# Kernel optimization log

Measured on AMD Instinct MI355X. Metric: run time of the kernel, lower is better.

The kernel has to match this reference:

```python
import jax, jax.numpy as jnp
import numpy as np

V, E, HL, HH, T_STEPS, N_STEPS = 32000, 768, 1024, 768, 5, 3
B, S = 8, 256
EPS = 1e-5


def _ln(x, g, b):
    m = jnp.mean(x, axis=-1, keepdims=True)
    v = jnp.var(x, axis=-1, keepdims=True)
    return (x - m) * jax.lax.rsqrt(v + EPS) * g + b


def _gru(x, h, Wi, bi, Wh, bh, lni_g, lni_b, lnh_g, lnh_b):
    # Wi: [3, in_dim, H]; gates stacked in order (r, z, n)
    xi = jnp.einsum('bd,kdh->kbh', x, Wi) + bi[:, None, :]
    hi = jnp.einsum('bh,khg->kbg', h, Wh) + bh[:, None, :]
    xi = _ln(xi, lni_g[:, None, :], lni_b[:, None, :])
    hi = _ln(hi, lnh_g[:, None, :], lnh_b[:, None, :])
    r = jax.nn.sigmoid(xi[0] + hi[0])
    z = jax.nn.sigmoid(xi[1] + hi[1])
    n = jnp.tanh(xi[2] + r * hi[2])
    return (1.0 - z) * n + z * h


def setup_inputs() -> dict:
    key = jax.random.key(0)
    ks = jax.random.split(key, 12)
    lin = E + HH  # low-level cell input dim (x concat h_h)

    def xavier(k, shape, fan_in, fan_out):
        lim = float(np.sqrt(6.0 / (fan_in + fan_out)))
        return jax.random.uniform(k, shape, jnp.float32, -lim, lim)

    inp = {
        'input_ids': jax.random.randint(ks[0], (B, S), 0, V),
        'emb': xavier(ks[1], (V, E), V, E),
        'ln_emb_g': jnp.ones((E,), jnp.float32),
        'ln_emb_b': jnp.zeros((E,), jnp.float32),
        'low_Wi': xavier(ks[2], (3, lin, HL), lin, HL),
        'low_bi': jnp.zeros((3, HL), jnp.float32),
        'low_Wh': xavier(ks[3], (3, HL, HL), HL, HL),
        'low_bh': jnp.zeros((3, HL), jnp.float32),
        'low_lni_g': jnp.ones((3, HL), jnp.float32),
        'low_lni_b': jnp.zeros((3, HL), jnp.float32),
        'low_lnh_g': jnp.ones((3, HL), jnp.float32),
        'low_lnh_b': jnp.zeros((3, HL), jnp.float32),
        'high_Wi': xavier(ks[4], (3, HL, HH), HL, HH),
        'high_bi': jnp.zeros((3, HH), jnp.float32),
        'high_Wh': xavier(ks[5], (3, HH, HH), HH, HH),
        'high_bh': jnp.zeros((3, HH), jnp.float32),
        'high_lni_g': jnp.ones((3, HH), jnp.float32),
        'high_lni_b': jnp.zeros((3, HH), jnp.float32),
        'high_lnh_g': jnp.ones((3, HH), jnp.float32),
        'high_lnh_b': jnp.zeros((3, HH), jnp.float32),
        'Wout': xavier(ks[6], (HH, V), HH, V),
        'bout': jnp.zeros((V,), jnp.float32),
    }
    return inp


def reference(input_ids, emb, ln_emb_g, ln_emb_b,
              low_Wi, low_bi, low_Wh, low_bh,
              low_lni_g, low_lni_b, low_lnh_g, low_lnh_b,
              high_Wi, high_bi, high_Wh, high_bh,
              high_lni_g, high_lni_b, high_lnh_g, high_lnh_b,
              Wout, bout):
    b = input_ids.shape[0]
    h_l0 = jnp.zeros((b, HL), jnp.float32)
    h_h0 = jnp.zeros((b, HH), jnp.float32)

    def step(carry, ids_t):
        h_l, h_h = carry
        x = _ln(emb[ids_t], ln_emb_g, ln_emb_b)  # [B, E]
        for _ in range(N_STEPS):
            for _ in range(T_STEPS):
                h_l = _gru(jnp.concatenate([x, h_h], axis=-1), h_l,
                           low_Wi, low_bi, low_Wh, low_bh,
                           low_lni_g, low_lni_b, low_lnh_g, low_lnh_b)
            h_h = _gru(h_l, h_h,
                       high_Wi, high_bi, high_Wh, high_bh,
                       high_lni_g, high_lni_b, high_lnh_g, high_lnh_b)
        logits_t = h_h @ Wout + bout  # [B, V]
        return (h_l, h_h), logits_t

    _, logits = jax.lax.scan(step, (h_l0, h_h0), input_ids.T)  # [S, B, V]
    return jnp.transpose(logits, (1, 0, 2))  # [B, S, V]
```

## Files before the change

kernel.cpp:

```cpp
#include <hip/hip_runtime.h>
#include <hip/hip_bf16.h>


#define NWG 128
#define NTH 256
#define EPSV 1e-5f
#define NROUND 4608

typedef __attribute__((ext_vector_type(4))) float f32x4;
typedef __attribute__((ext_vector_type(8))) short short8;
typedef unsigned long long u64;

struct PArgs {
  const int* ids; const float* emb; const float* lng; const float* lnb;
  const float* lWi; const float* lbi; const float* lWh; const float* lbh;
  const float* llig; const float* llib; const float* llhg; const float* llhb;
  const float* hWi; const float* hbi; const float* hWh; const float* hbh;
  const float* hlig; const float* hlib; const float* hlhg; const float* hlhb;
  int* arr; int* rel; int* cnt; u64* sredG; u64* statsG; float* hlR; float* hhR;
  __hip_bfloat16* hist; float* WiT; float* hWiT; float* hWhT;
};

__device__ __forceinline__ float sigm(float x) { return 1.f / (1.f + __expf(-x)); }
__device__ __forceinline__ float tanh_f(float x) {
  x = fminf(15.f, fmaxf(-15.f, x));
  float e = __expf(2.f * x);
  return (e - 1.f) / (e + 1.f);
}
__device__ __forceinline__ int aldi(const int* p) {
  return __hip_atomic_load(p, __ATOMIC_RELAXED, __HIP_MEMORY_SCOPE_AGENT);
}
__device__ __forceinline__ u64 aldu(const u64* p) {
  return __hip_atomic_load(p, __ATOMIC_RELAXED, __HIP_MEMORY_SCOPE_AGENT);
}
__device__ __forceinline__ void asti(int* p, int v) {
  __hip_atomic_store(p, v, __ATOMIC_RELAXED, __HIP_MEMORY_SCOPE_AGENT);
}
__device__ __forceinline__ u64 pk2(float a, float b) {
  union { u64 u; float f[2]; } c; c.f[0] = a; c.f[1] = b; return c.u;
}
__device__ __forceinline__ void astu(u64* p, u64 v) {
  __hip_atomic_store(p, v, __ATOMIC_RELAXED, __HIP_MEMORY_SCOPE_AGENT);
}
__device__ __forceinline__ void ast(float* p, float v) {
  __hip_atomic_store(p, v, __ATOMIC_RELAXED, __HIP_MEMORY_SCOPE_AGENT);
}
__device__ __forceinline__ void ald4x8(const float* p0, const float* p1,
                                       const float* p2, const float* p3,
                                       const float* p4, const float* p5,
                                       const float* p6, const float* p7,
                                       float4& a, float4& b, float4& c, float4& d,
                                       float4& e, float4& f, float4& g, float4& h) {
  asm volatile(
      "global_load_dwordx4 %0, %8, off sc1\n\t"
      "global_load_dwordx4 %1, %9, off sc1\n\t"
      "global_load_dwordx4 %2, %10, off sc1\n\t"
      "global_load_dwordx4 %3, %11, off sc1\n\t"
      "global_load_dwordx4 %4, %12, off sc1\n\t"
      "global_load_dwordx4 %5, %13, off sc1\n\t"
      "global_load_dwordx4 %6, %14, off sc1\n\t"
      "global_load_dwordx4 %7, %15, off sc1\n\t"
      "s_waitcnt vmcnt(0)"
      : "=&v"(a), "=&v"(b), "=&v"(c), "=&v"(d),
        "=&v"(e), "=&v"(f), "=&v"(g), "=&v"(h)
      : "v"(p0), "v"(p1), "v"(p2), "v"(p3),
        "v"(p4), "v"(p5), "v"(p6), "v"(p7)
      : "memory");
}
__device__ __forceinline__ void ald4x4(const float* p0, const float* p1,
                                       const float* p2, const float* p3,
                                       float4& a, float4& b, float4& c, float4& d) {
  asm volatile(
      "global_load_dwordx4 %0, %4, off sc1\n\t"
      "global_load_dwordx4 %1, %5, off sc1\n\t"
      "global_load_dwordx4 %2, %6, off sc1\n\t"
      "global_load_dwordx4 %3, %7, off sc1\n\t"
      "s_waitcnt vmcnt(0)"
      : "=&v"(a), "=&v"(b), "=&v"(c), "=&v"(d)
      : "v"(p0), "v"(p1), "v"(p2), "v"(p3)
      : "memory");
}
__device__ __forceinline__ void ald4x3(const float* p0, const float* p1,
                                       const float* p2,
                                       float4& a, float4& b, float4& c) {
  asm volatile(
      "global_load_dwordx4 %0, %3, off sc1\n\t"
      "global_load_dwordx4 %1, %4, off sc1\n\t"
      "global_load_dwordx4 %2, %5, off sc1\n\t"
      "s_waitcnt vmcnt(0)"
      : "=&v"(a), "=&v"(b), "=&v"(c)
      : "v"(p0), "v"(p1), "v"(p2)
      : "memory");
}

__global__ void __launch_bounds__(NTH) hrm_recur(PArgs P) {
  __shared__ float WhS[24 * 1024];
  __shared__ float Bb[8 * 1024];
  __shared__ float XW[24 * 8];
  __shared__ float xiNs[24 * 8];
  __shared__ float stg[2 * 24 * 8];
  __shared__ float sred[96];
  __shared__ float xm[8], xrs[8];
  __shared__ float mbuf[96][4];
  __shared__ int idsh[8];
  __shared__ int okf;

  const int tid = threadIdx.x;

  if (blockIdx.x >= NWG) {
    const int pl = blockIdx.x - NWG;
    #pragma unroll 1
    for (int r = 1; r <= NROUND; ++r) {
      if (tid < 64) {
        const u64* ap = (const u64*)(P.arr + pl * 128) + tid;
        int lim = 1 << 22, g1 = 1;
        for (;;) {
          u64 v = aldu(ap);
          int a0 = (int)(unsigned)(v & 0xffffffffull);
          int a1 = (int)(unsigned)(v >> 32);
          if (__all(a0 >= r && a1 >= r)) break;
          if (--lim == 0) { g1 = 0; break; }
          __builtin_amdgcn_s_sleep(1);
        }
        if (tid == 0) okf = g1;
      }
      __syncthreads();
      if (!okf) {
        if (tid < 8) asti(P.rel + pl * 128 + tid * 16, 1 << 30);
        return;
      }
      const int ph = (r - 1) % 6;
      const bool full = (ph == 0 || ph == 5);
      const int lo = pl * 24 + (full ? 0 : 12);
      const int n  = full ? 24 : 12;
      const float invD = (ph == 5) ? (1.f / 768.f) : (1.f / 1024.f);
      const int par = r & 1;
      if (tid < (n >> 1) * 8) {
        int rp = (lo >> 1) + (tid >> 3), q = tid & 7;
        const float* fb = (const float*)(P.statsG + (size_t)par * 128 * 48);
        float4 s; s.x = 0.f; s.y = 0.f; s.z = 0.f; s.w = 0.f;
        #pragma unroll
        for (int blk = 0; blk < 2; ++blk) {
          int w0 = q * 16 + blk * 8;
          float4 t0,t1,t2,t3,t4,t5,t6,t7;
          ald4x8(fb + (size_t)(w0+0)*96 + rp*4, fb + (size_t)(w0+1)*96 + rp*4,
                 fb + (size_t)(w0+2)*96 + rp*4, fb + (size_t)(w0+3)*96 + rp*4,
                 fb + (size_t)(w0+4)*96 + rp*4, fb + (size_t)(w0+5)*96 + rp*4,
                 fb + (size_t)(w0+6)*96 + rp*4, fb + (size_t)(w0+7)*96 + rp*4,
                 t0,t1,t2,t3,t4,t5,t6,t7);
          s.x += t0.x+t1.x+t2.x+t3.x+t4.x+t5.x+t6.x+t7.x;
          s.y += t0.y+t1.y+t2.y+t3.y+t4.y+t5.y+t6.y+t7.y;
          s.z += t0.z+t1.z+t2.z+t3.z+t4.z+t5.z+t6.z+t7.z;
          s.w += t0.w+t1.w+t2.w+t3.w+t4.w+t5.w+t6.w+t7.w;
        }
        mbuf[tid][0] = s.x; mbuf[tid][1] = s.y; mbuf[tid][2] = s.z; mbuf[tid][3] = s.w;
      }
      __syncthreads();
      if (tid < n) {
        int rpl = tid >> 1, comp = tid & 1;
        float s1 = 0.f, s2 = 0.f;
        #pragma unroll
        for (int q = 0; q < 8; ++q) {
          s1 += mbuf[rpl * 8 + q][comp * 2 + 0];
          s2 += mbuf[rpl * 8 + q][comp * 2 + 1];
        }
        float m = s1 * invD;
        float rs = rsqrtf(s2 * invD - m * m + EPSV);
        astu(P.sredG + (size_t)pl * 96 + (size_t)par * 48 + lo + tid, pk2(m, rs));
      }
      asm volatile("s_waitcnt vmcnt(0)" ::: "memory");
      __syncthreads();
      if (tid < 8) asti(P.rel + pl * 128 + tid * 16, r);
    }
    return;
  }

  const int wg = blockIdx.x;
  const int ks = tid & 31, cg = tid >> 5;
  const int lj8 = wg * 8, lj6 = wg * 6;
  const int rep = wg & 3;

  auto arriveA = [&](int pl, int r) {
    asm volatile("s_waitcnt vmcnt(0)" ::: "memory");
    __syncthreads();
    if (tid == 0) asti(P.arr + pl * 128 + wg, r);
  };
  auto pollRel = [&](int pl, int r, bool full) -> bool {
    if (tid == 0) {
      const int* rp = P.rel + pl * 128 + (wg & 7) * 16;
      int lim = 1 << 22, v = 0;
      do {
        v = aldi(rp);
        if (v >= r) break;
        __builtin_amdgcn_s_sleep(1);
      } while (--lim);
      okf = (lim != 0 && v < (1 << 29)) ? 1 : 0;
    }
    __syncthreads();
    if (okf) {
      int lo = pl * 24 + (full ? 0 : 12);
      int n  = full ? 24 : 12;
      if (tid < n) {
        int row = lo + tid;
        union { u64 u; float f[2]; } c;
        c.u = aldu(P.sredG + (size_t)pl * 96 + (size_t)(r & 1) * 48 + row);
        int local = row - pl * 24;
        int set = local / 12, rem = local % 12, g = rem >> 2, bq = rem & 3;
        int b = pl * 4 + bq;
        sred[set * 48 + g * 16 + b * 2] = c.f[0];
        sred[set * 48 + g * 16 + b * 2 + 1] = c.f[1];
      }
      __syncthreads();
    }
    return okf != 0;
  };
  auto waitB = [&](int pl, int target) -> bool {
    if (tid < 64) {
      bool active = tid < 8;
      const int* cp = P.cnt + pl * 256 + (size_t)(active ? tid : 0) * 32;
      int lim = 1 << 22;
      for (;;) {
        int v = active ? aldi(cp) : 0;
        int sum = v;
        sum += __shfl_xor(sum, 1);
        sum += __shfl_xor(sum, 2);
        sum += __shfl_xor(sum, 4);
        int total = __shfl(sum, 0);
        if (total >= target) break;
        if (--lim == 0) break;
        __builtin_amdgcn_s_sleep(2);
      }
      if (tid == 0) okf = (lim != 0) ? 1 : 0;
    }
    __syncthreads();
    return okf != 0;
  };
  auto gate_commit = [&](int pl) {
    asm volatile("s_waitcnt vmcnt(0)" ::: "memory");
    if (tid == 0)
      __hip_atomic_fetch_add(P.cnt + pl * 256 + (size_t)(wg & 7) * 32, 1,
                             __ATOMIC_RELAXED, __HIP_MEMORY_SCOPE_AGENT);
  };

  auto stage_hl = [&](int pl) {
    const float* base = P.hlR + (size_t)rep * 8192 + (size_t)pl * 4096 + tid * 4;
    float4 t0,t1,t2,t3;
    ald4x4(base + 0*1024, base + 1*1024, base + 2*1024, base + 3*1024,
           t0,t1,t2,t3);
    float* db = &Bb[pl * 4096 + tid * 4];
    *(float4*)&db[0*1024] = t0; *(float4*)&db[1*1024] = t1;
    *(float4*)&db[2*1024] = t2; *(float4*)&db[3*1024] = t3;
  };
  auto stage_hh = [&](int pl) {
    const float* base = P.hhR + (size_t)rep * 6144 + (size_t)pl * 3072;
    int bi[3], ki[3];
    #pragma unroll
    for (int i = 0; i < 3; ++i) {
      int c = i * 256 + tid; int bq = c / 192; int k = (c - bq * 192) * 4;
      bi[i] = bq; ki[i] = k;
    }
    float4 t0,t1,t2;
    ald4x3(base + bi[0]*768 + ki[0], base + bi[1]*768 + ki[1],
           base + bi[2]*768 + ki[2], t0,t1,t2);
    *(float4*)&Bb[(pl*4+bi[0])*1024 + ki[0]] = t0;
    *(float4*)&Bb[(pl*4+bi[1])*1024 + ki[1]] = t1;
    *(float4*)&Bb[(pl*4+bi[2])*1024 + ki[2]] = t2;
  };

  auto gemm_lowh = [&](int pl, float (&acc)[3][4]) {
    const int c0 = cg * 3;
    const float* w0p = &WhS[(c0 + 0) * 1024];
    const float* w1p = &WhS[(c0 + 1) * 1024];
    const float* w2p = &WhS[(c0 + 2) * 1024];
    const float* hb = &Bb[pl * 4096];
    #pragma unroll
    for (int i = 0; i < 8; ++i) {
      int k = i * 128 + ks * 4;
      float4 w0 = *(const float4*)&w0p[k];
      float4 w1 = *(const float4*)&w1p[k];
      float4 w2 = *(const float4*)&w2p[k];
      #pragma unroll
      for (int bq = 0; bq < 4; ++bq) {
        float4 h = *(const float4*)&hb[bq * 1024 + k];
        acc[0][bq] += w0.x*h.x + w0.y*h.y + w0.z*h.z + w0.w*h.w;
        acc[1][bq] += w1.x*h.x + w1.y*h.y + w1.z*h.z + w1.w*h.w;
        acc[2][bq] += w2.x*h.x + w2.y*h.y + w2.z*h.z + w2.w*h.w;
      }
    }
  };
  auto gemm_xih = [&](int pl, float (&acc)[3][4]) {
    const float* wp[3];
    #pragma unroll
    for (int cc = 0; cc < 3; ++cc) {
      int c = cg * 3 + cc; int g = c >> 3, jj = c & 7;
      wp[cc] = P.WiT + ((size_t)g * 1024 + lj8 + jj) * 1536 + 768;
    }
    const float* hb = &Bb[pl * 4096];
    #pragma unroll
    for (int i = 0; i < 6; ++i) {
      int k = i * 128 + ks * 4;
      float4 w0 = *(const float4*)&wp[0][k];
      float4 w1 = *(const float4*)&wp[1][k];
      float4 w2 = *(const float4*)&wp[2][k];
      #pragma unroll
      for (int bq = 0; bq < 4; ++bq) {
        float4 h = *(const float4*)&hb[bq * 1024 + k];
        acc[0][bq] += w0.x*h.x + w0.y*h.y + w0.z*h.z + w0.w*h.w;
        acc[1][bq] += w1.x*h.x + w1.y*h.y + w1.z*h.z + w1.w*h.w;
        acc[2][bq] += w2.x*h.x + w2.y*h.y + w2.z*h.z + w2.w*h.w;
      }
    }
  };
  auto gemm_hxi = [&](int pl, float (&acc)[3][4]) {
    if (cg >= 6) return;
    const float* wp[3];
    #pragma unroll
    for (int cc = 0; cc < 3; ++cc) {
      int c = cg * 3 + cc; int g = c / 6, jj = c % 6;
      wp[cc] = P.hWiT + ((size_t)g * 768 + lj6 + jj) * 1024;
    }
    const float* hb = &Bb[pl * 4096];
    #pragma unroll
    for (int i = 0; i < 8; ++i) {
      int k = i * 128 + ks * 4;
      float4 w0 = *(const float4*)&wp[0][k];
      float4 w1 = *(const float4*)&wp[1][k];
      float4 w2 = *(const float4*)&wp[2][k];
      #pragma unroll
      for (int bq = 0; bq < 4; ++bq) {
        float4 h = *(const float4*)&hb[bq * 1024 + k];
        acc[0][bq] += w0.x*h.x + w0.y*h.y + w0.z*h.z + w0.w*h.w;
        acc[1][bq] += w1.x*h.x + w1.y*h.y + w1.z*h.z + w1.w*h.w;
        acc[2][bq] += w2.x*h.x + w2.y*h.y + w2.z*h.z + w2.w*h.w;
      }
    }
  };
  auto gemm_hhh = [&](int pl, float (&acc)[3][4]) {
    if (cg >= 6) return;
    const float* wp[3];
    #pragma unroll
    for (int cc = 0; cc < 3; ++cc) {
      int c = cg * 3 + cc; int g = c / 6, jj = c % 6;
      wp[cc] = P.hWhT + ((size_t)g * 768 + lj6 + jj) * 768;
    }
    const float* hb = &Bb[pl * 4096];
    #pragma unroll
    for (int i = 0; i < 6; ++i) {
      int k = i * 128 + ks * 4;
      float4 w0 = *(const float4*)&wp[0][k];
      float4 w1 = *(const float4*)&wp[1][k];
      float4 w2 = *(const float4*)&wp[2][k];
      #pragma unroll
      for (int bq = 0; bq < 4; ++bq) {
        float4 h = *(const float4*)&hb[bq * 1024 + k];
        acc[0][bq] += w0.x*h.x + w0.y*h.y + w0.z*h.z + w0.w*h.w;
        acc[1][bq] += w1.x*h.x + w1.y*h.y + w1.z*h.z + w1.w*h.w;
        acc[2][bq] += w2.x*h.x + w2.y*h.y + w2.z*h.z + w2.w*h.w;
      }
    }
  };

  auto redstage = [&](int pl, float (&acc)[3][4], int set, const float* bias,
                      int dim, int perg, int jb, bool addXW) {
    #pragma unroll
    for (int cc = 0; cc < 3; ++cc)
      #pragma unroll
      for (int bq = 0; bq < 4; ++bq) {
        float v = acc[cc][bq];
        #pragma unroll
        for (int m = 1; m < 32; m <<= 1) v += __shfl_xor(v, m, 64);
        acc[cc][bq] = v;
      }
    if ((tid & 31) == 0) {
      int cgl = tid >> 5;
      #pragma unroll
      for (int cc = 0; cc < 3; ++cc) {
        int c = cgl * 3 + cc;
        if (c < perg * 3) {
          int g = (perg == 8) ? (c >> 3) : (c / 6);
          int jj = (perg == 8) ? (c & 7) : (c % 6);
          float bs = bias[g * dim + jb + jj];
          #pragma unroll
          for (int bq = 0; bq < 4; ++bq) {
            float v = acc[cc][bq] + bs;
            if (addXW) v += XW[c * 8 + pl * 4 + bq];
            stg[set * 192 + c * 8 + pl * 4 + bq] = v;
          }
        }
      }
    }
  };

  auto stats_put = [&](int pl, int par, int set, int perg) {
    if (tid < 12) {
      int g = tid >> 2, bq = tid & 3;
      float s1 = 0.f, s2 = 0.f;
      for (int jj = 0; jj < perg; ++jj) {
        float v = stg[set * 192 + (g * perg + jj) * 8 + pl * 4 + bq];
        s1 += v; s2 += v * v;
      }
      int row = pl * 24 + set * 12 + g * 4 + bq;
      astu(P.statsG + ((size_t)par * 128 + wg) * 48 + row, pk2(s1, s2));
    }
  };

  auto gate_low = [&](int pl, bool isA) {
    if (tid < 32) {
      int jj = tid & 7, bq = tid >> 3; int b = pl * 4 + bq; int j = lj8 + jj;
      float xin[3], hin[3];
      #pragma unroll
      for (int g = 0; g < 3; ++g) {
        int c = g * 8 + jj;
        if (isA) {
          float m = sred[g * 16 + b * 2], rs = sred[g * 16 + b * 2 + 1];
          float v = (stg[c * 8 + b] - m) * rs * P.llig[g * 1024 + j] + P.llib[g * 1024 + j];
          xiNs[c * 8 + b] = v; xin[g] = v;
        } else {
          xin[g] = xiNs[c * 8 + b];
        }
        float m2 = sred[48 + g * 16 + b * 2], rs2 = sred[48 + g * 16 + b * 2 + 1];
        hin[g] = (stg[192 + c * 8 + b] - m2) * rs2 * P.llhg[g * 1024 + j] + P.llhb[g * 1024 + j];
      }
      float rg = sigm(xin[0] + hin[0]);
      float zg = sigm(xin[1] + hin[1]);
      float ng = tanh_f(xin[2] + rg * hin[2]);
      float hold = Bb[b * 1024 + j];
      float hv = (1.f - zg) * ng + zg * hold;
      #pragma unroll
      for (int rp = 0; rp < 4; ++rp) ast(&P.hlR[rp * 8192 + b * 1024 + j], hv);
    }
  };

  auto gate_high = [&](int pl, int t, int nn) {
    if (tid < 24) {
      int jj = tid % 6, bq = tid / 6; int b = pl * 4 + bq; int j = lj6 + jj;
      float xin[3], hin[3];
      #pragma unroll
      for (int g = 0; g < 3; ++g) {
        int c = g * 6 + jj;
        float m = sred[g * 16 + b * 2], rs = sred[g * 16 + b * 2 + 1];
        xin[g] = (stg[c * 8 + b] - m) * rs * P.hlig[g * 768 + j] + P.hlib[g * 768 + j];
        float m2 = sred[48 + g * 16 + b * 2], rs2 = sred[48 + g * 16 + b * 2 + 1];
        hin[g] = (stg[192 + c * 8 + b] - m2) * rs2 * P.hlhg[g * 768 + j] + P.hlhb[g * 768 + j];
      }
      float rg = sigm(xin[0] + hin[0]);
      float zg = sigm(xin[1] + hin[1]);
      float ng = tanh_f(xin[2] + rg * hin[2]);
      float hold = Bb[b * 1024 + j];
      float hv = (1.f - zg) * ng + zg * hold;
      #pragma unroll
      for (int rp = 0; rp < 4; ++rp) ast(&P.hhR[rp * 6144 + b * 768 + j], hv);
      if (nn == 2) P.hist[((size_t)t * 8 + b) * 768 + j] = __float2bfloat16(hv);
    }
  };

  auto xfun = [&](int tt) {
    int bq = tid >> 5, u = tid & 31;
    if (tid < 8) idsh[tid] = P.ids[tid * 256 + tt];
    int id = P.ids[bq * 256 + tt];
    const float* e = P.emb + (size_t)id * 768;
    float s1 = 0.f, s2 = 0.f;
    #pragma unroll
    for (int q = 0; q < 24; q += 4) {
      float4 v = *(const float4*)&e[u * 24 + q];
      s1 += v.x + v.y + v.z + v.w;
      s2 += v.x*v.x + v.y*v.y + v.z*v.z + v.w*v.w;
    }
    #pragma unroll
    for (int m = 1; m < 32; m <<= 1) { s1 += __shfl_xor(s1, m, 64); s2 += __shfl_xor(s2, m, 64); }
    if (u == 0) { float mm = s1 / 768.f; xm[bq] = mm; xrs[bq] = rsqrtf(s2 / 768.f - mm * mm + EPSV); }
    __syncthreads();
    float acc[3][8] = {};
    const float* wp[3];
    #pragma unroll
    for (int cc = 0; cc < 3; ++cc) {
      int c = cg * 3 + cc; int g = c >> 3, jj = c & 7;
      wp[cc] = P.WiT + ((size_t)g * 1024 + lj8 + jj) * 1536;
    }
    int idv[8];
    #pragma unroll
    for (int bb = 0; bb < 8; ++bb) idv[bb] = idsh[bb];
    #pragma unroll
    for (int i = 0; i < 6; ++i) {
      int k = i * 128 + ks * 4;
      float4 w0 = *(const float4*)&wp[0][k];
      float4 w1 = *(const float4*)&wp[1][k];
      float4 w2 = *(const float4*)&wp[2][k];
      float4 gam = *(const float4*)&P.lng[k];
      float4 bet = *(const float4*)&P.lnb[k];
      #pragma unroll
      for (int bb = 0; bb < 8; ++bb) {
        float4 xv = *(const float4*)&P.emb[(size_t)idv[bb] * 768 + k];
        float4 xn;
        xn.x = (xv.x - xm[bb]) * xrs[bb] * gam.x + bet.x;
        xn.y = (xv.y - xm[bb]) * xrs[bb] * gam.y + bet.y;
        xn.z = (xv.z - xm[bb]) * xrs[bb] * gam.z + bet.z;
        xn.w = (xv.w - xm[bb]) * xrs[bb] * gam.w + bet.w;
        acc[0][bb] += w0.x*xn.x + w0.y*xn.y + w0.z*xn.z + w0.w*xn.w;
        acc[1][bb] += w1.x*xn.x + w1.y*xn.y + w1.z*xn.z + w1.w*xn.w;
        acc[2][bb] += w2.x*xn.x + w2.y*xn.y + w2.z*xn.z + w2.w*xn.w;
      }
    }
    #pragma unroll
    for (int cc = 0; cc < 3; ++cc)
      #pragma unroll
      for (int bb = 0; bb < 8; ++bb) {
        float v = acc[cc][bb];
        #pragma unroll
        for (int m = 1; m < 32; m <<= 1) v += __shfl_xor(v, m, 64);
        acc[cc][bb] = v;
      }
    if ((tid & 31) == 0) {
      int cgl = tid >> 5;
      #pragma unroll
      for (int cc = 0; cc < 3; ++cc)
        #pragma unroll
        for (int bb = 0; bb < 8; ++bb)
          XW[(cgl * 3 + cc) * 8 + bb] = acc[cc][bb];
    }
    __syncthreads();
  };

  #pragma unroll 1
  for (int g = 0; g < 3; ++g)
    for (int it = 0; it < 6; ++it) {
      int k = it * 256 + tid;
      const float* src = P.lWi + ((size_t)g * 1536 + k) * 1024 + lj8;
      float4 v0 = *(const float4*)src; float4 v1 = *(const float4*)(src + 4);
      float vv[8] = {v0.x, v0.y, v0.z, v0.w, v1.x, v1.y, v1.z, v1.w};
      for (int jj = 0; jj < 8; ++jj)
        P.WiT[((size_t)g * 1024 + lj8 + jj) * 1536 + k] = vv[jj];
    }
  #pragma unroll 1
  for (int g = 0; g < 3; ++g)
    for (int it = 0; it < 4; ++it) {
      int k = it * 256 + tid;
      const float* src = P.hWi + ((size_t)g * 1024 + k) * 768 + lj6;
      float2 a = *(const float2*)src, b2v = *(const float2*)(src + 2), c2v = *(const float2*)(src + 4);
      float vv[6] = {a.x, a.y, b2v.x, b2v.y, c2v.x, c2v.y};
      for (int jj = 0; jj < 6; ++jj)
        P.hWiT[((size_t)g * 768 + lj6 + jj) * 1024 + k] = vv[jj];
    }
  #pragma unroll 1
  for (int g = 0; g < 3; ++g)
    for (int it = 0; it < 3; ++it) {
      int k = it * 256 + tid;
      const float* src = P.hWh + ((size_t)g * 768 + k) * 768 + lj6;
      float2 a = *(const float2*)src, b2v = *(const float2*)(src + 2), c2v = *(const float2*)(src + 4);
      float vv[6] = {a.x, a.y, b2v.x, b2v.y, c2v.x, c2v.y};
      for (int jj = 0; jj < 6; ++jj)
        P.hWhT[((size_t)g * 768 + lj6 + jj) * 768 + k] = vv[jj];
    }
  #pragma unroll 1
  for (int g = 0; g < 3; ++g)
    for (int it = 0; it < 4; ++it) {
      int k = it * 256 + tid;
      const float* src = P.lWh + ((size_t)g * 1024 + k) * 1024 + lj8;
      float4 v0 = *(const float4*)src; float4 v1 = *(const float4*)(src + 4);
      float vv[8] = {v0.x, v0.y, v0.z, v0.w, v1.x, v1.y, v1.z, v1.w};
      for (int jj = 0; jj < 8; ++jj) WhS[(g * 8 + jj) * 1024 + k] = vv[jj];
    }
  __syncthreads();
  xfun(0);

  int r = 1;
  bool alive = true;
  #pragma unroll 1
  for (int t = 0; t < 256 && alive; ++t) {
    #pragma unroll 1
    for (int nn = 0; nn < 3 && alive; ++nn) {
      {
        #pragma unroll 1
        for (int pl = 0; pl < 2; ++pl) {
          alive = waitB(pl, NWG * (r - 1)); if (!alive) break;
          stage_hh(pl); __syncthreads();
          float aX[3][4] = {};
          gemm_xih(pl, aX);
          redstage(pl, aX, 0, P.lbi, 1024, 8, lj8, true);
          __syncthreads();
          stage_hl(pl); __syncthreads();
          float aH[3][4] = {};
          gemm_lowh(pl, aH);
          redstage(pl, aH, 1, P.lbh, 1024, 8, lj8, false);
          __syncthreads();
          stats_put(pl, r & 1, 0, 8); stats_put(pl, r & 1, 1, 8);
          arriveA(pl, r);
        }
        if (!alive) break;
        #pragma unroll 1
        for (int pl = 0; pl < 2; ++pl) {
          alive = pollRel(pl, r, true); if (!alive) break;
          gate_low(pl, true);
          gate_commit(pl);
        }
        if (!alive) break;
        ++r;
      }
      #pragma unroll 1
      for (int it = 1; it < 5 && alive; ++it) {
        #pragma unroll 1
        for (int pl = 0; pl < 2; ++pl) {
          alive = waitB(pl, NWG * (r - 1)); if (!alive) break;
          stage_hl(pl); __syncthreads();
          float a2[3][4] = {};
          gemm_lowh(pl, a2);
          redstage(pl, a2, 1, P.lbh, 1024, 8, lj8, false);
          __syncthreads();
          stats_put(pl, r & 1, 1, 8);
          arriveA(pl, r);
        }
        if (!alive) break;
        #pragma unroll 1
        for (int pl = 0; pl < 2; ++pl) {
          alive = pollRel(pl, r, false); if (!alive) break;
          gate_low(pl, false);
          gate_commit(pl);
        }
        if (!alive) break;
        ++r;
      }
      if (!alive) break;
      {
        #pragma unroll 1
        for (int pl = 0; pl < 2; ++pl) {
          alive = waitB(pl, NWG * (r - 1)); if (!alive) break;
          stage_hl(pl); __syncthreads();
          float aX[3][4] = {};
          gemm_hxi(pl, aX);
          redstage(pl, aX, 0, P.hbi, 768, 6, lj6, false);
          __syncthreads();
          stage_hh(pl); __syncthreads();
          float aH[3][4] = {};
          gemm_hhh(pl, aH);
          redstage(pl, aH, 1, P.hbh, 768, 6, lj6, false);
          __syncthreads();
          stats_put(pl, r & 1, 0, 6); stats_put(pl, r & 1, 1, 6);
          arriveA(pl, r);
        }
        if (!alive) break;
        #pragma unroll 1
        for (int pl = 0; pl < 2; ++pl) {
          alive = pollRel(pl, r, true); if (!alive) break;
          gate_high(pl, t, nn);
          gate_commit(pl);
        }
        if (!alive) break;
        ++r;
        if (nn == 2 && t < 255) { __syncthreads(); xfun(t + 1); }
      }
    }
  }
}

__global__ void __launch_bounds__(256) wout_t(const float* __restrict__ W,
                                              __hip_bfloat16* __restrict__ WT) {
  __shared__ float T[64][65];
  int n0 = blockIdx.x * 64, k0 = blockIdx.y * 64;
  int tid = threadIdx.x;
  int lane16 = tid & 15, grp = tid >> 4;
  #pragma unroll
  for (int i = 0; i < 4; ++i) {
    int kl = i * 16 + grp; int nl = lane16 * 4;
    float4 v = *(const float4*)&W[(size_t)(k0 + kl) * 32000 + n0 + nl];
    T[kl][nl] = v.x; T[kl][nl + 1] = v.y; T[kl][nl + 2] = v.z; T[kl][nl + 3] = v.w;
  }
  __syncthreads();
  #pragma unroll
  for (int i = 0; i < 4; ++i) {
    int nl = i * 16 + grp; int kl = lane16 * 4;
    union { ushort4 v; __hip_bfloat16 h[4]; } u;
    for (int q = 0; q < 4; ++q) u.h[q] = __float2bfloat16(T[kl + q][nl]);
    *(ushort4*)&WT[(size_t)(n0 + nl) * 768 + k0 + kl] = u.v;
  }
}

__global__ void __launch_bounds__(256) logits_gemm(const __hip_bfloat16* __restrict__ Ah,
                                                   const __hip_bfloat16* __restrict__ Bt,
                                                   const float* __restrict__ bias,
                                                   float* __restrict__ out) {
  __shared__ short As[128 * 64];
  __shared__ short Bs[128 * 64];
  int m0 = blockIdx.y * 128, n0 = blockIdx.x * 128;
  int tid = threadIdx.x, lane = tid & 63, w = tid >> 6;
  int wr = w >> 1, wc = w & 1;
  int r16 = lane & 15, khalf = (lane >> 4) * 8;
  f32x4 acc[4][4];
  #pragma unroll
  for (int i = 0; i < 4; ++i)
    #pragma unroll
    for (int j = 0; j < 4; ++j)
      #pragma unroll
      for (int q = 0; q < 4; ++q) acc[i][j][q] = 0.f;

  for (int kt = 0; kt < 12; ++kt) {
    int k0 = kt * 64;
    __syncthreads();
    #pragma unroll
    for (int it = 0; it < 4; ++it) {
      int f = it * 2048 + tid * 8; int row = f >> 6, col = f & 63;
      *(uint4*)&As[f] = *(const uint4*)&Ah[(size_t)(m0 + row) * 768 + k0 + col];
      *(uint4*)&Bs[f] = *(const uint4*)&Bt[(size_t)(n0 + row) * 768 + k0 + col];
    }
    __syncthreads();
    #pragma unroll
    for (int kk = 0; kk < 64; kk += 32) {
      short8 af[4], bfr[4];
      #pragma unroll
      for (int i = 0; i < 4; ++i)
        af[i] = *(short8*)&As[(wr * 64 + i * 16 + r16) * 64 + kk + khalf];
      #pragma unroll
      for (int j = 0; j < 4; ++j)
        bfr[j] = *(short8*)&Bs[(wc * 64 + j * 16 + r16) * 64 + kk + khalf];
      #pragma unroll
      for (int i = 0; i < 4; ++i)
        #pragma unroll
        for (int j = 0; j < 4; ++j)
          acc[i][j] = __builtin_amdgcn_mfma_f32_16x16x32_bf16(af[i], bfr[j], acc[i][j], 0, 0, 0);
    }
  }
  #pragma unroll
  for (int i = 0; i < 4; ++i)
    #pragma unroll
    for (int j = 0; j < 4; ++j)
      #pragma unroll
      for (int q = 0; q < 4; ++q) {
        int m = m0 + wr * 64 + i * 16 + ((lane >> 4) * 4 + q);
        int n = n0 + wc * 64 + j * 16 + (lane & 15);
        out[(size_t)(m & 7) * 8192000 + (size_t)(m >> 3) * 32000 + n] =
            acc[i][j][q] + bias[n];
      }
}

extern "C" void kernel_launch(void* const* d_in, const int* in_sizes, int n_in,
                              void* d_out, int out_size, void* d_ws, size_t ws_size,
                              hipStream_t stream) {
  (void)in_sizes; (void)n_in; (void)out_size; (void)ws_size;
  char* wsb = (char*)d_ws;
  size_t off = 0;
  auto take = [&](size_t bytes) -> void* {
    void* p = wsb + off;
    off += (bytes + 1023) & ~(size_t)1023;
    return p;
  };
  int* arr    = (int*)take((size_t)2 * 128 * 4);
  int* rel    = (int*)take((size_t)2 * 128 * 4);
  int* cnt    = (int*)take((size_t)2 * 8 * 32 * 4);
  u64* sredG  = (u64*)take((size_t)2 * 2 * 48 * 8);
  float* hlR  = (float*)take((size_t)4 * 8 * 1024 * 4);
  float* hhR  = (float*)take((size_t)4 * 8 * 768 * 4);
  size_t state_bytes = off;
  u64* statsG = (u64*)take((size_t)2 * 128 * 48 * 8);
  __hip_bfloat16* hist = (__hip_bfloat16*)take((size_t)2048 * 768 * 2);
  float* WiT  = (float*)take((size_t)3 * 1024 * 1536 * 4);
  float* hWiT = (float*)take((size_t)3 * 768 * 1024 * 4);
  float* hWhT = (float*)take((size_t)3 * 768 * 768 * 4);
  __hip_bfloat16* WoutT = (__hip_bfloat16*)take((size_t)32000 * 768 * 2);

  hipMemsetAsync(d_ws, 0, state_bytes, stream);

  wout_t<<<dim3(500, 12), 256, 0, stream>>>((const float*)d_in[20], WoutT);

  PArgs A;
  A.ids = (const int*)d_in[0];   A.emb = (const float*)d_in[1];
  A.lng = (const float*)d_in[2]; A.lnb = (const float*)d_in[3];
  A.lWi = (const float*)d_in[4]; A.lbi = (const float*)d_in[5];
  A.lWh = (const float*)d_in[6]; A.lbh = (const float*)d_in[7];
  A.llig = (const float*)d_in[8];  A.llib = (const float*)d_in[9];
  A.llhg = (const float*)d_in[10]; A.llhb = (const float*)d_in[11];
  A.hWi = (const float*)d_in[12];  A.hbi = (const float*)d_in[13];
  A.hWh = (const float*)d_in[14];  A.hbh = (const float*)d_in[15];
  A.hlig = (const float*)d_in[16]; A.hlib = (const float*)d_in[17];
  A.hlhg = (const float*)d_in[18]; A.hlhb = (const float*)d_in[19];
  A.arr = arr; A.rel = rel; A.cnt = cnt; A.sredG = sredG; A.statsG = statsG;
  A.hlR = hlR; A.hhR = hhR;
  A.hist = hist; A.WiT = WiT; A.hWiT = hWiT; A.hWhT = hWhT;

  hrm_recur<<<NWG + 2, NTH, 0, stream>>>(A);

  logits_gemm<<<dim3(250, 16), 256, 0, stream>>>(hist, WoutT,
                                                 (const float*)d_in[21],
                                                 (float*)d_out);
}
```

Measured before the change: 59.90 ms.

## Software-pipeline the two batch planes across rounds to overlap compute with barrier waits

Flattens the nested t/nn/iteration loops into one round loop with a phase index. The work of the two independent planes is staggered: plane 1's GEMM runs while plane 0's release is pending, and plane 0's next-round GEMM is issued before plane 1's gate. The goal is to hide the cross-workgroup barrier latency of one plane behind the compute of the other. The schedule of xfun (embedding prep) moves to before the next round's plane-0 compute, which adds risk in the ordering of shared-memory reuse.

```diff
diff --git a/kernel.cpp b/kernel.cpp
--- a/kernel.cpp
+++ b/kernel.cpp
@@ -563,92 +563,67 @@
   __syncthreads();
   xfun(0);
 
-  int r = 1;
+  auto do_compute = [&](int pl, int r) {
+    int ph = (r - 1) % 6;
+    if (ph == 0) {
+      stage_hh(pl); __syncthreads();
+      float aX[3][4] = {};
+      gemm_xih(pl, aX);
+      redstage(pl, aX, 0, P.lbi, 1024, 8, lj8, true);
+      __syncthreads();
+      stage_hl(pl); __syncthreads();
+      float aH[3][4] = {};
+      gemm_lowh(pl, aH);
+      redstage(pl, aH, 1, P.lbh, 1024, 8, lj8, false);
+      __syncthreads();
+      stats_put(pl, r & 1, 0, 8); stats_put(pl, r & 1, 1, 8);
+    } else if (ph != 5) {
+      stage_hl(pl); __syncthreads();
+      float a2[3][4] = {};
+      gemm_lowh(pl, a2);
+      redstage(pl, a2, 1, P.lbh, 1024, 8, lj8, false);
+      __syncthreads();
+      stats_put(pl, r & 1, 1, 8);
+    } else {
+      stage_hl(pl); __syncthreads();
+      float aX[3][4] = {};
+      gemm_hxi(pl, aX);
+      redstage(pl, aX, 0, P.hbi, 768, 6, lj6, false);
+      __syncthreads();
+      stage_hh(pl); __syncthreads();
+      float aH[3][4] = {};
+      gemm_hhh(pl, aH);
+      redstage(pl, aH, 1, P.hbh, 768, 6, lj6, false);
+      __syncthreads();
+      stats_put(pl, r & 1, 0, 6); stats_put(pl, r & 1, 1, 6);
+    }
+    arriveA(pl, r);
+  };
+  auto do_gate = [&](int pl, int r) {
+    int ph = (r - 1) % 6;
+    if (ph != 5) gate_low(pl, ph == 0);
+    else gate_high(pl, (r - 1) / 18, ((r - 1) / 6) % 3);
+  };
+
   bool alive = true;
+  do_compute(0, 1);
   #pragma unroll 1
-  for (int t = 0; t < 256 && alive; ++t) {
-    #pragma unroll 1
-    for (int nn = 0; nn < 3 && alive; ++nn) {
-      {
-        #pragma unroll 1
-        for (int pl = 0; pl < 2; ++pl) {
-          alive = waitB(pl, NWG * (r - 1)); if (!alive) break;
-          stage_hh(pl); __syncthreads();
-          float aX[3][4] = {};
-          gemm_xih(pl, aX);
-          redstage(pl, aX, 0, P.lbi, 1024, 8, lj8, true);
-          __syncthreads();
-          stage_hl(pl); __syncthreads();
-          float aH[3][4] = {};
-          gemm_lowh(pl, aH);
-          redstage(pl, aH, 1, P.lbh, 1024, 8, lj8, false);
-          __syncthreads();
-          stats_put(pl, r & 1, 0, 8); stats_put(pl, r & 1, 1, 8);
-          arriveA(pl, r);
-        }
-        if (!alive) break;
-        #pragma unroll 1
-        for (int pl = 0; pl < 2; ++pl) {
-          alive = pollRel(pl, r, true); if (!alive) break;
-          gate_low(pl, true);
-          gate_commit(pl);
-        }
-        if (!alive) break;
-        ++r;
-      }
-      #pragma unroll 1
-      for (int it = 1; it < 5 && alive; ++it) {
-        #pragma unroll 1
-        for (int pl = 0; pl < 2; ++pl) {
-          alive = waitB(pl, NWG * (r - 1)); if (!alive) break;
-          stage_hl(pl); __syncthreads();
-          float a2[3][4] = {};
-          gemm_lowh(pl, a2);
-          redstage(pl, a2, 1, P.lbh, 1024, 8, lj8, false);
-          __syncthreads();
-          stats_put(pl, r & 1, 1, 8);
-          arriveA(pl, r);
-        }
-        if (!alive) break;
-        #pragma unroll 1
-        for (int pl = 0; pl < 2; ++pl) {
-          alive = pollRel(pl, r, false); if (!alive) break;
-          gate_low(pl, false);
-          gate_commit(pl);
-        }
-        if (!alive) break;
-        ++r;
-      }
-      if (!alive) break;
-      {
-        #pragma unroll 1
-        for (int pl = 0; pl < 2; ++pl) {
-          alive = waitB(pl, NWG * (r - 1)); if (!alive) break;
-          stage_hl(pl); __syncthreads();
-          float aX[3][4] = {};
-          gemm_hxi(pl, aX);
-          redstage(pl, aX, 0, P.hbi, 768, 6, lj6, false);
-          __syncthreads();
-          stage_hh(pl); __syncthreads();
-          float aH[3][4] = {};
-          gemm_hhh(pl, aH);
-          redstage(pl, aH, 1, P.hbh, 768, 6, lj6, false);
-          __syncthreads();
-          stats_put(pl, r & 1, 0, 6); stats_put(pl, r & 1, 1, 6);
-          arriveA(pl, r);
-        }
-        if (!alive) break;
-        #pragma unroll 1
-        for (int pl = 0; pl < 2; ++pl) {
-          alive = pollRel(pl, r, true); if (!alive) break;
-          gate_high(pl, t, nn);
-          gate_commit(pl);
-        }
-        if (!alive) break;
-        ++r;
-        if (nn == 2 && t < 255) { __syncthreads(); xfun(t + 1); }
-      }
-    }
+  for (int r = 1; r <= NROUND && alive; ++r) {
+    const int ph = (r - 1) % 6;
+    const bool full = (ph == 0 || ph == 5);
+    alive = waitB(1, NWG * (r - 1)); if (!alive) break;
+    do_compute(1, r);
+    alive = pollRel(0, r, full); if (!alive) break;
+    do_gate(0, r);
+    gate_commit(0);
+    if (r < NROUND) {
+      alive = waitB(0, NWG * r); if (!alive) break;
+      if (r % 18 == 0) xfun(r / 18);
+      do_compute(0, r + 1);
+    }
+    alive = pollRel(1, r, full); if (!alive) break;
+    do_gate(1, r);
+    gate_commit(1);
   }
 }
 
```

New measurement: 74.32 ms. +24.1%, slower.
